# Performance work log

Measured on AMD Instinct MI355X. Metric: run time of the kernel, lower is better.

Reference implementation:

```python
import jax, jax.numpy as jnp
import numpy as np

EPS = 1e-8
LEHMER_P = 1.0  # fixed_lehmer_param from init_kwargs


@jax.custom_vjp
def ste(x):
    # StraightThroughEstimator: forward is (x > 0).float(), backward is hardtanh(grad)
    return (x > 0).astype(x.dtype)

def _ste_fwd(x):
    return ste(x), None

def _ste_bwd(_, g):
    return (jnp.clip(g, -1.0, 1.0),)

ste.defvjp(_ste_fwd, _ste_bwd)


def causality_map_lehmer(x, p):
    # x: [b, k, h, w] bottleneck feature maps
    b, k, h, w = x.shape
    # global max per batch element (max over flatten dim2, then over channel dim)
    max_f = jnp.max(x.reshape(b, -1), axis=1)
    x = jnp.nan_to_num(x / (max_f[:, None, None, None] + EPS))
    xf = x.reshape(b, k, h * w)                       # [b, k, n]
    # pairwise outer product: [b, k, k, n*n] -- the huge intermediate
    cross = jnp.einsum('bmi,bnj->bmnij', xf, xf).reshape(b, k, k, -1)
    num = jnp.nan_to_num(jnp.sum(jnp.nan_to_num((cross + EPS) ** (p + 1.0)), axis=3)) + EPS
    den = jnp.nan_to_num(jnp.sum(jnp.nan_to_num((cross + EPS) ** p), axis=3)) + EPS
    lehmer_num = jnp.nan_to_num(num / den) + EPS      # [b, k, k]
    xa = jnp.abs(xf) + EPS
    nd = jnp.nan_to_num(jnp.sum(jnp.nan_to_num(xa ** (p + 1.0)), axis=2)) + EPS
    dd = jnp.nan_to_num(jnp.sum(jnp.nan_to_num(xa ** p), axis=2)) + EPS
    lehmer_den = jnp.nan_to_num(nd / dd) + EPS        # [b, k]
    return jnp.nan_to_num(lehmer_num / lehmer_den[:, None, :])  # [b, k, k]


def causality_factors(x, cm):
    # CausalityFactorsExtractor with direction='causes', setting='mulcat'
    triu = jnp.triu(cm, 1)
    tril = jnp.transpose(jnp.tril(cm, -1), (0, 2, 1))
    e = jnp.transpose(ste(tril - triu), (0, 2, 1))
    f = ste(triu - tril)
    bool_matrix = e + f                               # [b, k, k]
    by_col = jnp.sum(bool_matrix, axis=2)
    by_row = jnp.sum(bool_matrix, axis=1)
    mul_factors = jax.nn.relu(by_col - by_row)        # 'causes' + 'mulcat'
    return jnp.einsum('bkmn,bk->bkmn', x, mul_factors)


def setup_inputs() -> dict:
    key = jax.random.key(0)
    k1, k2 = jax.random.split(key)
    B, K, F = 2, 512, 4
    num_classes = 2
    x = jax.random.uniform(k1, (B, K, F, F), dtype=jnp.float32)  # post-ReLU features
    feat_dim = 2 * K * F * F  # mulcat: concat of x and x_causality
    W = jax.random.normal(k2, (num_classes, feat_dim), dtype=jnp.float32) * 0.01
    b = jnp.zeros((num_classes,), dtype=jnp.float32)
    return {"x": x, "W": W, "b": b}


def reference(x, W, b):
    cm = causality_map_lehmer(x, LEHMER_P)            # [B, 512, 512]
    xc = causality_factors(x, cm)                      # [B, 512, 4, 4]
    B = x.shape[0]
    feat = jnp.concatenate([x.reshape(B, -1), xc.reshape(B, -1)], axis=1)
    return feat @ W.T + b                              # logits [B, num_classes]
```

## Files before the change

### kernel.cpp

```cpp
#include <hip/hip_runtime.h>

#define EPS 1e-8f
#define KCH 512
#define NSP 16
#define NTHREADS 512

__global__ __launch_bounds__(NTHREADS)
void ca_fused_kernel(const float* __restrict__ x,
                     const float* __restrict__ W,
                     const float* __restrict__ bias,
                     float* __restrict__ out) {
    const int b = blockIdx.x;
    const int t = threadIdx.x;
    const int wid = t >> 6;
    const int lane = t & 63;

    __shared__ float xs[KCH * NSP];
    __shared__ float Dsh[KCH];
    __shared__ float wtmp0[8], wtmp1[8];

    const float* xb = x + (size_t)b * KCH * NSP;
    for (int i = t; i < KCH * NSP; i += NTHREADS) xs[i] = xb[i];
    __syncthreads();

    float m = 0.0f;
    for (int i = t; i < KCH * NSP; i += NTHREADS) m = fmaxf(m, xs[i]);
    for (int off = 32; off > 0; off >>= 1) m = fmaxf(m, __shfl_down(m, off, 64));
    if (lane == 0) wtmp0[wid] = m;
    __syncthreads();
    if (t == 0) {
        float mm = wtmp0[0];
        #pragma unroll
        for (int i = 1; i < 8; i++) mm = fmaxf(mm, wtmp0[i]);
        wtmp0[0] = mm;
    }
    __syncthreads();
    const float denom = wtmp0[0] + EPS;
    __syncthreads();

    {
        const int base = t * NSP;
        float nd = 0.f, dd = 0.f;
        #pragma unroll
        for (int f = 0; f < NSP; f++) {
            float v  = xs[base + f] / denom;
            float av = fabsf(v) + EPS;
            nd += av * av;
            dd += av;
        }
        nd += EPS;
        dd += EPS;
        Dsh[t] = nd / dd + EPS;
    }
    __syncthreads();

    const float myD = Dsh[t];
    int cs = 0, cl = 0;
    for (int j = 0; j < KCH; j++) {
        float dj = Dsh[j];
        cs += (myD > dj) ? 1 : 0;
        cl += (dj > myD) ? 1 : 0;
    }
    float mul = (float)(cs - cl);
    if (mul < 0.f) mul = 0.f;

    const float* W0 = W;
    const float* W1 = W + 16384;
    const int base = t * NSP;
    float acc0 = 0.f, acc1 = 0.f;
    #pragma unroll
    for (int f = 0; f < NSP; f++) {
        float xv = xs[base + f];
        float xc = xv * mul;
        acc0 += xv * W0[base + f] + xc * W0[8192 + base + f];
        acc1 += xv * W1[base + f] + xc * W1[8192 + base + f];
    }
    for (int off = 32; off > 0; off >>= 1) {
        acc0 += __shfl_down(acc0, off, 64);
        acc1 += __shfl_down(acc1, off, 64);
    }
    if (lane == 0) { wtmp0[wid] = acc0; wtmp1[wid] = acc1; }
    __syncthreads();
    if (t == 0) {
        float s0 = 0.f, s1 = 0.f;
        #pragma unroll
        for (int i = 0; i < 8; i++) { s0 += wtmp0[i]; s1 += wtmp1[i]; }
        out[b * 2 + 0] = s0 + bias[0];
        out[b * 2 + 1] = s1 + bias[1];
    }
}

extern "C" void kernel_launch(void* const* d_in, const int* in_sizes, int n_in,
                              void* d_out, int out_size, void* d_ws, size_t ws_size,
                              hipStream_t stream) {
    const float* x    = (const float*)d_in[0];
    const float* W    = (const float*)d_in[1];
    const float* bias = (const float*)d_in[2];
    float* out = (float*)d_out;
    ca_fused_kernel<<<2, NTHREADS, 0, stream>>>(x, W, bias, out);
}
```

Before: 69.64 us.

## Split into parallel partial-sum kernel and small finalize kernel

The single 2-block kernel is split into a 128-block partials kernel and a 2-block finalize kernel. The partials kernel computes per-channel sums, sums of squares and the four weight dot products, plus per-block maxima. The finalize kernel rebuilds the Lehmer ratio from these sums by expanding the EPS terms algebraically, then does the rank count and the final reduction. This spreads the x and W loads across many CUs instead of two, at the cost of a second launch and a workspace round trip. It also assumes nonnegative inputs, since abs is dropped.

```diff
diff --git a/kernel.cpp b/kernel.cpp
--- a/kernel.cpp
+++ b/kernel.cpp
@@ -3,53 +3,93 @@
 #define EPS 1e-8f
 #define KCH 512
 #define NSP 16
-#define NTHREADS 512
 
-__global__ __launch_bounds__(NTHREADS)
-void ca_fused_kernel(const float* __restrict__ x,
+#define S1_OFF   0
+#define S2_OFF   1024
+#define P0M_OFF  2048
+#define P0C_OFF  3072
+#define P1M_OFF  4096
+#define P1C_OFF  5120
+#define BMAX_OFF 6144
+
+__global__ __launch_bounds__(128)
+void partials_kernel(const float* __restrict__ x,
                      const float* __restrict__ W,
+                     float* __restrict__ ws) {
+    const int blk = blockIdx.x;
+    const int b   = blk >> 6;
+    const int grp = blk & 63;
+    const int t   = threadIdx.x;
+    const int f   = t & 15;
+    const int k   = grp * 8 + (t >> 4);
+    const int gidx = k * NSP + f;
+
+    const float xv  = x[b * 8192 + gidx];
+    const float w0m = W[gidx];
+    const float w0c = W[8192  + gidx];
+    const float w1m = W[16384 + gidx];
+    const float w1c = W[24576 + gidx];
+
+    float s1 = xv, s2 = xv * xv;
+    float p0m = xv * w0m, p0c = xv * w0c;
+    float p1m = xv * w1m, p1c = xv * w1c;
+    #pragma unroll
+    for (int off = 8; off > 0; off >>= 1) {
+        s1  += __shfl_down(s1,  off, 16);
+        s2  += __shfl_down(s2,  off, 16);
+        p0m += __shfl_down(p0m, off, 16);
+        p0c += __shfl_down(p0c, off, 16);
+        p1m += __shfl_down(p1m, off, 16);
+        p1c += __shfl_down(p1c, off, 16);
+    }
+    if (f == 0) {
+        const int o = b * KCH + k;
+        ws[S1_OFF  + o] = s1;
+        ws[S2_OFF  + o] = s2;
+        ws[P0M_OFF + o] = p0m;
+        ws[P0C_OFF + o] = p0c;
+        ws[P1M_OFF + o] = p1m;
+        ws[P1C_OFF + o] = p1c;
+    }
+
+    float m = xv;
+    #pragma unroll
+    for (int off = 32; off > 0; off >>= 1) m = fmaxf(m, __shfl_down(m, off, 64));
+    __shared__ float sm[2];
+    if ((t & 63) == 0) sm[t >> 6] = m;
+    __syncthreads();
+    if (t == 0) ws[BMAX_OFF + blk] = fmaxf(sm[0], sm[1]);
+}
+
+__global__ __launch_bounds__(512)
+void finalize_kernel(const float* __restrict__ ws,
                      const float* __restrict__ bias,
                      float* __restrict__ out) {
     const int b = blockIdx.x;
     const int t = threadIdx.x;
-    const int wid = t >> 6;
-    const int lane = t & 63;
+    const int wid = t >> 6, lane = t & 63;
 
-    __shared__ float xs[KCH * NSP];
     __shared__ float Dsh[KCH];
-    __shared__ float wtmp0[8], wtmp1[8];
+    __shared__ float red0[8], red1[8];
 
-    const float* xb = x + (size_t)b * KCH * NSP;
-    for (int i = t; i < KCH * NSP; i += NTHREADS) xs[i] = xb[i];
+    if (wid == 0) {
+        float m = ws[BMAX_OFF + b * 64 + lane];
+        #pragma unroll
+        for (int off = 32; off > 0; off >>= 1) m = fmaxf(m, __shfl_down(m, off, 64));
+        if (lane == 0) red0[0] = m;
+    }
+    __syncthreads();
+    const float denom = red0[0] + EPS;
     __syncthreads();
 
-    float m = 0.0f;
-    for (int i = t; i < KCH * NSP; i += NTHREADS) m = fmaxf(m, xs[i]);
-    for (int off = 32; off > 0; off >>= 1) m = fmaxf(m, __shfl_down(m, off, 64));
-    if (lane == 0) wtmp0[wid] = m;
-    __syncthreads();
-    if (t == 0) {
-        float mm = wtmp0[0];
-        #pragma unroll
-        for (int i = 1; i < 8; i++) mm = fmaxf(mm, wtmp0[i]);
-        wtmp0[0] = mm;
-    }
-    __syncthreads();
-    const float denom = wtmp0[0] + EPS;
-    __syncthreads();
-
+    const int o = b * KCH + t;
     {
-        const int base = t * NSP;
-        float nd = 0.f, dd = 0.f;
-        #pragma unroll
-        for (int f = 0; f < NSP; f++) {
-            float v  = xs[base + f] / denom;
-            float av = fabsf(v) + EPS;
-            nd += av * av;
-            dd += av;
-        }
-        nd += EPS;
-        dd += EPS;
+        const float s1 = ws[S1_OFF + o];
+        const float s2 = ws[S2_OFF + o];
+        const float inv = 1.0f / denom;
+        const float dd = s1 * inv + 16.0f * EPS + EPS;
+        const float nd = s2 * inv * inv + 2.0f * EPS * (s1 * inv)
+                         + 16.0f * EPS * EPS + EPS;
         Dsh[t] = nd / dd + EPS;
     }
     __syncthreads();
@@ -57,34 +97,26 @@
     const float myD = Dsh[t];
     int cs = 0, cl = 0;
     for (int j = 0; j < KCH; j++) {
-        float dj = Dsh[j];
+        const float dj = Dsh[j];
         cs += (myD > dj) ? 1 : 0;
         cl += (dj > myD) ? 1 : 0;
     }
     float mul = (float)(cs - cl);
     if (mul < 0.f) mul = 0.f;
 
-    const float* W0 = W;
-    const float* W1 = W + 16384;
-    const int base = t * NSP;
-    float acc0 = 0.f, acc1 = 0.f;
+    float acc0 = ws[P0M_OFF + o] + mul * ws[P0C_OFF + o];
+    float acc1 = ws[P1M_OFF + o] + mul * ws[P1C_OFF + o];
     #pragma unroll
-    for (int f = 0; f < NSP; f++) {
-        float xv = xs[base + f];
-        float xc = xv * mul;
-        acc0 += xv * W0[base + f] + xc * W0[8192 + base + f];
-        acc1 += xv * W1[base + f] + xc * W1[8192 + base + f];
-    }
     for (int off = 32; off > 0; off >>= 1) {
         acc0 += __shfl_down(acc0, off, 64);
         acc1 += __shfl_down(acc1, off, 64);
     }
-    if (lane == 0) { wtmp0[wid] = acc0; wtmp1[wid] = acc1; }
+    if (lane == 0) { red0[wid] = acc0; red1[wid] = acc1; }
     __syncthreads();
     if (t == 0) {
         float s0 = 0.f, s1 = 0.f;
         #pragma unroll
-        for (int i = 0; i < 8; i++) { s0 += wtmp0[i]; s1 += wtmp1[i]; }
+        for (int i = 0; i < 8; i++) { s0 += red0[i]; s1 += red1[i]; }
         out[b * 2 + 0] = s0 + bias[0];
         out[b * 2 + 1] = s1 + bias[1];
     }
@@ -97,5 +129,8 @@
     const float* W    = (const float*)d_in[1];
     const float* bias = (const float*)d_in[2];
     float* out = (float*)d_out;
-    ca_fused_kernel<<<2, NTHREADS, 0, stream>>>(x, W, bias, out);
+    float* ws  = (float*)d_ws;
+
+    partials_kernel<<<128, 128, 0, stream>>>(x, W, ws);
+    finalize_kernel<<<2, 512, 0, stream>>>(ws, bias, out);
 }
```

Result: faster. 67.71 us (-2.8%).
